# Optimization experiments

Hardware: AMD Instinct MI355X
Metric: run time of the kernel (lower is better)

The kernel has to match this reference:

```python
import jax, jax.numpy as jnp
from jax import lax
import numpy as np

B, T, I, H, L, O = 256, 200, 32, 512, 2, 7
EPS = 1e-12


def setup_inputs() -> dict:
    key = jax.random.key(0)
    ks = jax.random.split(key, 11)
    s = 0.05
    return {
        "x": jax.random.normal(ks[0], (B, T, I), dtype=jnp.float32),
        "w_ih0": jax.random.normal(ks[1], (4 * H, I), dtype=jnp.float32) * s,
        "w_hh0": jax.random.normal(ks[2], (4 * H, H), dtype=jnp.float32) * s,
        "b_ih0": jax.random.normal(ks[3], (4 * H,), dtype=jnp.float32) * s,
        "b_hh0": jax.random.normal(ks[4], (4 * H,), dtype=jnp.float32) * s,
        "w_ih1": jax.random.normal(ks[5], (4 * H, H), dtype=jnp.float32) * s,
        "w_hh1": jax.random.normal(ks[6], (4 * H, H), dtype=jnp.float32) * s,
        "b_ih1": jax.random.normal(ks[7], (4 * H,), dtype=jnp.float32) * s,
        "b_hh1": jax.random.normal(ks[8], (4 * H,), dtype=jnp.float32) * s,
        "w_fc": jax.random.normal(ks[9], (O, H), dtype=jnp.float32) * s,
        "b_fc": jax.random.normal(ks[10], (O,), dtype=jnp.float32) * s,
    }


def _lstm_layer(x_tbi, w_ih, w_hh, b_ih, b_hh):
    # x_tbi: [T, B, in]; PyTorch gate order i, f, g, o
    b = b_ih + b_hh
    hdim = w_hh.shape[1]
    batch = x_tbi.shape[1]
    # precompute input projections for all timesteps (one big GEMM)
    xg = jnp.einsum('tbi,gi->tbg', x_tbi, w_ih) + b  # [T, B, 4H]

    def step(carry, xgt):
        h, c = carry
        g = xgt + h @ w_hh.T
        i, f, gg, o = jnp.split(g, 4, axis=-1)
        c = jax.nn.sigmoid(f) * c + jax.nn.sigmoid(i) * jnp.tanh(gg)
        h = jax.nn.sigmoid(o) * jnp.tanh(c)
        return (h, c), h

    h0 = jnp.zeros((batch, hdim), x_tbi.dtype)
    (_, _), hs = lax.scan(step, (h0, h0), xg)
    return hs  # [T, B, H]


def reference(x, w_ih0, w_hh0, b_ih0, b_hh0, w_ih1, w_hh1, b_ih1, b_hh1, w_fc, b_fc):
    xt = jnp.transpose(x, (1, 0, 2))  # [T, B, I]
    h1 = _lstm_layer(xt, w_ih0, w_hh0, b_ih0, b_hh0)
    h2 = _lstm_layer(h1, w_ih1, w_hh1, b_ih1, b_hh1)
    last = h2[-1]  # [B, H] = output[:, -1, :]
    y = last @ w_fc.T + b_fc  # [B, O]
    p = jax.nn.sigmoid(y[:, :3])
    rt = jnp.tanh(y[:, 3:])
    # F.normalize(p=2, dim=1, eps=1e-12)
    r = rt / jnp.maximum(jnp.linalg.norm(rt, axis=1, keepdims=True), EPS)
    return (p, r)
```

## Files before the change

kernel.cpp:

```cpp
#include <hip/hip_runtime.h>
#include <hip/hip_bf16.h>

#define TSEQ  200
#define BATCH 256
#define INDIM 32
#define HID   512
#define GATES 2048

typedef __bf16 bf16x8 __attribute__((ext_vector_type(8)));
typedef float  f32x4  __attribute__((ext_vector_type(4)));
typedef unsigned long long u64;

static constexpr size_t OFF_PW_IH0 = 0;
static constexpr size_t OFF_PW_HH0 = 0x20000;
static constexpr size_t OFF_PW_IH1 = 0x220000;
static constexpr size_t OFF_PW_HH1 = 0x420000;
static constexpr size_t OFF_B0     = 0x620000;
static constexpr size_t OFF_B1     = 0x622000;
static constexpr size_t OFF_H1     = 0x624000;
static constexpr size_t OFF_H2     = 0x724000;
static constexpr size_t OFF_CTR    = 0x7A4000;
static constexpr size_t OFF_H2P    = 0x7A6000;
static constexpr size_t ZERO_OFF   = OFF_H1;
static constexpr size_t ZERO_LEN   = OFF_H2P + 0x80000 - OFF_H1;

__device__ __forceinline__ float sigm(float v) { return 1.f / (1.f + __expf(-v)); }

__device__ __forceinline__ float tanh_fast(float v) {
    float e = __expf(-2.0f * fabsf(v));
    float t = (1.0f - e) / (1.0f + e);
    return copysignf(t, v);
}

__device__ __forceinline__ bf16x8 as_bf16x8(f32x4 v) {
    union { f32x4 f; bf16x8 b; } u; u.f = v; return u.b;
}

__device__ __forceinline__ bf16x8 load16_coh(const bf16x8* p) {
    bf16x8 v;
    asm volatile("global_load_dwordx4 %0, %1, off sc0 sc1"
                 : "=v"(v) : "v"(p) : "memory");
    return v;
}

__device__ __forceinline__ void store16_coh(void* p, u64 v0, u64 v1) {
    union { u64 u[2]; f32x4 f; } cv; cv.u[0] = v0; cv.u[1] = v1;
    asm volatile("global_store_dwordx4 %0, %1, off sc0 sc1"
                 :: "v"(p), "v"(cv.f) : "memory");
}

__device__ __forceinline__ unsigned load_flag_coh(const unsigned* p) {
    unsigned v;
    asm volatile("global_load_dword %0, %1, off sc0 sc1\n\t"
                 "s_waitcnt vmcnt(0)"
                 : "=v"(v) : "v"(p) : "memory");
    return v;
}

__global__ void pack_w(const float* __restrict__ W, __bf16* __restrict__ out, int ktlog2)
{
    int tid = blockIdx.x * 256 + threadIdx.x;
    int K = 32 << ktlog2;
    int j    = tid & 7;
    int lane = (tid >> 3) & 63;
    int rest = tid >> 9;
    int kt   = rest & ((1 << ktlog2) - 1);
    int r2   = rest >> ktlog2;
    int lnt  = r2 & 7;
    int bn   = r2 >> 3;
    int type = lnt >> 1, half = lnt & 1;
    int g    = type * 512 + bn * 32 + half * 16 + (lane & 15);
    int kcol = kt * 32 + (lane >> 4) * 8 + j;
    out[tid] = (__bf16)W[g * K + kcol];
}

__global__ void bias_comb(const float* __restrict__ a0, const float* __restrict__ a1,
                          const float* __restrict__ a2, const float* __restrict__ a3,
                          float* __restrict__ o0, float* __restrict__ o1)
{
    int tid = blockIdx.x * 256 + threadIdx.x;
    if (tid < GATES) { o0[tid] = a0[tid] + a1[tid]; o1[tid] = a2[tid] + a3[tid]; }
}

__global__ __launch_bounds__(256, 1) void lstm_persist(const float* __restrict__ x,
                                                       const float* __restrict__ wfc,
                                                       const float* __restrict__ bfc,
                                                       char* __restrict__ ws,
                                                       float* __restrict__ out)
{
    const int layer = blockIdx.x >> 7;
    const int lb    = blockIdx.x & 127;
    const int mtp   = lb >> 4;
    const int bn    = lb & 15;
    const int wid   = threadIdx.x >> 6;
    const int half  = wid & 1;
    const int kh    = wid >> 1;
    const int lane  = threadIdx.x & 63;
    const int q     = lane >> 4;
    const int c16   = lane & 15;
    unsigned* flg   = (unsigned*)(ws + OFF_CTR) + (size_t)mtp * 64;

    __shared__ float  red[2][64][33];
    __shared__ __bf16 htr[1024];
    __shared__ bf16x8 stg[2][2][16][64];

    const float* bias = (const float*)(ws + (layer ? OFF_B1 : OFF_B0));
    const int hidx = bn * 32 + half * 16 + c16;
    const float bi  = bias[hidx];
    const float bff = bias[512 + hidx];
    const float bg  = bias[1024 + hidx];
    const float bo  = bias[1536 + hidx];

    const bf16x8* __restrict__ pBx = (const bf16x8*)(ws + OFF_PW_IH0);
    const bf16x8* __restrict__ pBh = (const bf16x8*)(ws + OFF_PW_HH0);
    const bf16x8* __restrict__ pB1 = (const bf16x8*)(ws + OFF_PW_IH1);
    const bf16x8* __restrict__ pB2 = (const bf16x8*)(ws + OFF_PW_HH1);
    float* __restrict__ h2p = (float*)(ws + OFF_H2P);

    f32x4 Bw[64];
    f32x4 Bx[4];
    if (layer == 0) {
        #pragma unroll
        for (int j = 0; j < 8; ++j)
            #pragma unroll
            for (int ty = 0; ty < 4; ++ty)
                Bw[j * 4 + ty] = *(const f32x4*)&pBh[((bn * 8 + ty * 2 + half) * 16 + kh * 8 + j) * 64 + lane];
        #pragma unroll
        for (int ty = 0; ty < 4; ++ty)
            Bx[ty] = *(const f32x4*)&pBx[(bn * 8 + ty * 2 + half) * 64 + lane];
    } else {
        const bf16x8* __restrict__ pW = kh ? pB2 : pB1;
        #pragma unroll
        for (int j = 0; j < 16; ++j)
            #pragma unroll
            for (int ty = 0; ty < 4; ++ty)
                Bw[j * 4 + ty] = *(const f32x4*)&pW[((bn * 8 + ty * 2 + half) * 16 + j) * 64 + lane];
    }

    float creg[8] = {0.f,0.f,0.f,0.f,0.f,0.f,0.f,0.f};

    for (int k = 0; k <= TSEQ; ++k) {
        const bool active = layer ? (k >= 1) : (k < TSEQ);
        if (active) {
            const int t = k - layer;
            f32x4 acc[2][4] = {};

            const size_t h1rd = OFF_H1 + (size_t)((k + 3) & 3) * 0x40000;

            if (layer == 0) {
                const bf16x8* __restrict__ pA = (const bf16x8*)(ws + h1rd);
                bf16x8 tmp0[8];
                #pragma unroll
                for (int j = 0; j < 8; ++j)
                    tmp0[j] = load16_coh(&pA[((mtp * 2 + half) * 16 + kh * 8 + j) * 64 + lane]);
                bf16x8 ax[2];
                if (kh == 0) {
                    #pragma unroll
                    for (int m = 0; m < 2; ++m) {
                        const int b = (mtp * 2 + m) * 16 + c16;
                        const float* xp = x + ((size_t)b * TSEQ + t) * INDIM + q * 8;
                        float4 xlo = *(const float4*)xp;
                        float4 xhi = *(const float4*)(xp + 4);
                        ax[m][0] = (__bf16)xlo.x; ax[m][1] = (__bf16)xlo.y;
                        ax[m][2] = (__bf16)xlo.z; ax[m][3] = (__bf16)xlo.w;
                        ax[m][4] = (__bf16)xhi.x; ax[m][5] = (__bf16)xhi.y;
                        ax[m][6] = (__bf16)xhi.z; ax[m][7] = (__bf16)xhi.w;
                    }
                }
                asm volatile("s_waitcnt vmcnt(0)" ::: "memory");
                __builtin_amdgcn_sched_barrier(0);
                #pragma unroll
                for (int j = 0; j < 8; ++j)
                    stg[kh][half][j][lane] = tmp0[j];
                __syncthreads();
                bf16x8 af[16];
                #pragma unroll
                for (int j = 0; j < 8; ++j) {
                    af[j]     = stg[kh][0][j][lane];
                    af[8 + j] = stg[kh][1][j][lane];
                }
                if (kh == 0) {
                    #pragma unroll
                    for (int m = 0; m < 2; ++m)
                        #pragma unroll
                        for (int ty = 0; ty < 4; ++ty)
                            acc[m][ty] = __builtin_amdgcn_mfma_f32_16x16x32_bf16(ax[m], as_bf16x8(Bx[ty]), acc[m][ty], 0, 0, 0);
                }
                #pragma unroll
                for (int j = 0; j < 8; ++j) {
                    #pragma unroll
                    for (int ty = 0; ty < 4; ++ty) {
                        acc[0][ty] = __builtin_amdgcn_mfma_f32_16x16x32_bf16(af[j],     as_bf16x8(Bw[j * 4 + ty]), acc[0][ty], 0, 0, 0);
                        acc[1][ty] = __builtin_amdgcn_mfma_f32_16x16x32_bf16(af[8 + j], as_bf16x8(Bw[j * 4 + ty]), acc[1][ty], 0, 0, 0);
                    }
                }
            } else {
                const bf16x8* __restrict__ pA = kh
                    ? (const bf16x8*)(ws + OFF_H2 + (size_t)((k + 1) & 1) * 0x40000)
                    : (const bf16x8*)(ws + h1rd);
                bf16x8 tmp[16];
                #pragma unroll
                for (int j = 0; j < 16; ++j)
                    tmp[j] = load16_coh(&pA[((mtp * 2 + half) * 16 + j) * 64 + lane]);
                asm volatile("s_waitcnt vmcnt(0)" ::: "memory");
                __builtin_amdgcn_sched_barrier(0);
                #pragma unroll
                for (int j = 0; j < 16; ++j)
                    stg[kh][half][j][lane] = tmp[j];
                __syncthreads();
                bf16x8 a0[16], a1[16];
                #pragma unroll
                for (int j = 0; j < 8; ++j) {
                    a0[j]     = stg[kh][0][j][lane];
                    a0[8 + j] = stg[kh][1][j][lane];
                    a1[j]     = stg[kh][0][8 + j][lane];
                    a1[8 + j] = stg[kh][1][8 + j][lane];
                }
                #pragma unroll
                for (int j = 0; j < 8; ++j) {
                    #pragma unroll
                    for (int ty = 0; ty < 4; ++ty) {
                        acc[0][ty] = __builtin_amdgcn_mfma_f32_16x16x32_bf16(a0[j],     as_bf16x8(Bw[j * 4 + ty]), acc[0][ty], 0, 0, 0);
                        acc[1][ty] = __builtin_amdgcn_mfma_f32_16x16x32_bf16(a0[8 + j], as_bf16x8(Bw[j * 4 + ty]), acc[1][ty], 0, 0, 0);
                    }
                }
                #pragma unroll
                for (int j = 0; j < 8; ++j) {
                    #pragma unroll
                    for (int ty = 0; ty < 4; ++ty) {
                        acc[0][ty] = __builtin_amdgcn_mfma_f32_16x16x32_bf16(a1[j],     as_bf16x8(Bw[(8 + j) * 4 + ty]), acc[0][ty], 0, 0, 0);
                        acc[1][ty] = __builtin_amdgcn_mfma_f32_16x16x32_bf16(a1[8 + j], as_bf16x8(Bw[(8 + j) * 4 + ty]), acc[1][ty], 0, 0, 0);
                    }
                }
            }

            if (kh == 1) {
                #pragma unroll
                for (int m = 0; m < 2; ++m)
                    #pragma unroll
                    for (int ty = 0; ty < 4; ++ty)
                        #pragma unroll
                        for (int r = 0; r < 4; ++r)
                            red[half][lane][m * 16 + ty * 4 + r] = acc[m][ty][r];
            }
            __syncthreads();

            if (kh == 0) {
                __bf16* __restrict__ hout = (__bf16*)(ws + (layer
                    ? OFF_H2 + (size_t)(k & 1) * 0x40000
                    : OFF_H1 + (size_t)(k & 3) * 0x40000));
                #pragma unroll
                for (int m = 0; m < 2; ++m) {
                    #pragma unroll
                    for (int r = 0; r < 4; ++r) {
                        float pi = acc[m][0][r] + red[half][lane][m * 16 + r]      + bi;
                        float pf = acc[m][1][r] + red[half][lane][m * 16 + 4 + r]  + bff;
                        float pg = acc[m][2][r] + red[half][lane][m * 16 + 8 + r]  + bg;
                        float po = acc[m][3][r] + red[half][lane][m * 16 + 12 + r] + bo;
                        float cn = sigm(pf) * creg[m * 4 + r] + sigm(pi) * tanh_fast(pg);
                        float hn = sigm(po) * tanh_fast(cn);
                        creg[m * 4 + r] = cn;
                        htr[half * 512 + (m * 16 + q * 4 + r) * 16 + c16] = (__bf16)hn;
                        if (layer == 1 && k == TSEQ) {
                            const int b = (mtp * 2 + m) * 16 + q * 4 + r;
                            __hip_atomic_store(&h2p[b * HID + hidx], hn,
                                               __ATOMIC_RELAXED, __HIP_MEMORY_SCOPE_AGENT);
                        }
                    }
                }
                const int bt   = lane >> 5;
                const int qa1  = (lane >> 4) & 1;
                const int b15r = lane & 15;
                const u64* lp = (const u64*)&htr[half * 512 + (bt * 16 + b15r) * 16 + qa1 * 8];
                u64 v0 = lp[0], v1 = lp[1];
                const int f = (((mtp * 2 + bt) * 16) + bn) * 64 + (half * 2 + qa1) * 16 + b15r;
                u64* gp = (u64*)hout + (size_t)f * 2;
                store16_coh(gp, v0, v1);
            }
        }

        asm volatile("s_waitcnt vmcnt(0)" ::: "memory");
        __syncthreads();
        if (threadIdx.x == 0)
            __hip_atomic_store(flg + layer * 16 + bn, (unsigned)(k + 1),
                               __ATOMIC_RELAXED, __HIP_MEMORY_SCOPE_AGENT);
        if (threadIdx.x < 32) {
            const int need = (layer == 0 && threadIdx.x >= 16 && k < TSEQ) ? (k - 1) : (k + 1);
            while ((int)load_flag_coh(flg + threadIdx.x) < need)
                __builtin_amdgcn_s_sleep(1);
        }
        __syncthreads();
    }

    if (threadIdx.x < 64) {
        const int b = mtp * 32 + layer * 16 + bn;
        const float* h = h2p + b * HID;
        float hv[8];
        #pragma unroll
        for (int j = 0; j < 8; ++j)
            hv[j] = __hip_atomic_load(&h[lane * 8 + j], __ATOMIC_RELAXED, __HIP_MEMORY_SCOPE_AGENT);
        float y[7];
        #pragma unroll
        for (int o = 0; o < 7; ++o) {
            const float* wrow = wfc + o * HID;
            float s = 0.f;
            #pragma unroll
            for (int j = 0; j < 8; ++j) s += hv[j] * wrow[lane * 8 + j];
            #pragma unroll
            for (int off = 32; off >= 1; off >>= 1) s += __shfl_down(s, off);
            y[o] = s;
        }
        if (lane == 0) {
            out[b * 3 + 0] = sigm(y[0] + bfc[0]);
            out[b * 3 + 1] = sigm(y[1] + bfc[1]);
            out[b * 3 + 2] = sigm(y[2] + bfc[2]);
            float r0 = tanh_fast(y[3] + bfc[3]);
            float r1 = tanh_fast(y[4] + bfc[4]);
            float r2 = tanh_fast(y[5] + bfc[5]);
            float r3 = tanh_fast(y[6] + bfc[6]);
            float n = sqrtf(r0 * r0 + r1 * r1 + r2 * r2 + r3 * r3);
            n = fmaxf(n, 1e-12f);
            out[768 + b * 4 + 0] = r0 / n;
            out[768 + b * 4 + 1] = r1 / n;
            out[768 + b * 4 + 2] = r2 / n;
            out[768 + b * 4 + 3] = r3 / n;
        }
    }
}

extern "C" void kernel_launch(void* const* d_in, const int* in_sizes, int n_in,
                              void* d_out, int out_size, void* d_ws, size_t ws_size,
                              hipStream_t stream)
{
    const float* x    = (const float*)d_in[0];
    const float* wih0 = (const float*)d_in[1];
    const float* whh0 = (const float*)d_in[2];
    const float* bih0 = (const float*)d_in[3];
    const float* bhh0 = (const float*)d_in[4];
    const float* wih1 = (const float*)d_in[5];
    const float* whh1 = (const float*)d_in[6];
    const float* bih1 = (const float*)d_in[7];
    const float* bhh1 = (const float*)d_in[8];
    const float* wfc  = (const float*)d_in[9];
    const float* bfc  = (const float*)d_in[10];
    char* ws = (char*)d_ws;

    hipMemsetAsync(ws + ZERO_OFF, 0, ZERO_LEN, stream);

    pack_w<<<256,  256, 0, stream>>>(wih0, (__bf16*)(ws + OFF_PW_IH0), 0);
    pack_w<<<4096, 256, 0, stream>>>(whh0, (__bf16*)(ws + OFF_PW_HH0), 4);
    pack_w<<<4096, 256, 0, stream>>>(wih1, (__bf16*)(ws + OFF_PW_IH1), 4);
    pack_w<<<4096, 256, 0, stream>>>(whh1, (__bf16*)(ws + OFF_PW_HH1), 4);
    bias_comb<<<8, 256, 0, stream>>>(bih0, bhh0, bih1, bhh1,
                                     (float*)(ws + OFF_B0), (float*)(ws + OFF_B1));

    lstm_persist<<<256, 256, 0, stream>>>(x, wfc, bfc, ws, (float*)d_out);
}
```

Baseline: 1.433 ms.

## Replace per-step global barrier with tagged-data dataflow sync between LSTM blocks

Drops the per-timestep all-block flag barrier. Each 8-byte granule of the exchanged hidden-state buffers now carries a 16-bit step tag, and consumers spin on the data itself until every tag matches the expected step. Flags survive only as a lighter consumer-progress check that throttles overwriting of the 4-slot ring buffers, and layer-1 reads of h2 now use a 4-slot ring. This is meant to remove the barrier's round-trip latency on the recurrent critical path. In exchange the payload grows by half, 64-bit atomic loads replace 128-bit loads, there is extra packing work, and the polling is more complex.

```diff
diff --git a/kernel.cpp b/kernel.cpp
--- a/kernel.cpp
+++ b/kernel.cpp
@@ -17,12 +17,13 @@
 static constexpr size_t OFF_PW_HH1 = 0x420000;
 static constexpr size_t OFF_B0     = 0x620000;
 static constexpr size_t OFF_B1     = 0x622000;
-static constexpr size_t OFF_H1     = 0x624000;
-static constexpr size_t OFF_H2     = 0x724000;
-static constexpr size_t OFF_CTR    = 0x7A4000;
-static constexpr size_t OFF_H2P    = 0x7A6000;
-static constexpr size_t ZERO_OFF   = OFF_H1;
-static constexpr size_t ZERO_LEN   = OFF_H2P + 0x80000 - OFF_H1;
+static constexpr size_t SLOT_SZ    = 0x60000;
+static constexpr size_t OFF_RH1    = 0x20000;
+static constexpr size_t OFF_RH2    = 0x1A0000;
+static constexpr size_t OFF_CTR    = 0x624000;
+static constexpr size_t OFF_H2P    = 0x626000;
+static constexpr size_t ZERO_OFF   = OFF_CTR;
+static constexpr size_t ZERO_LEN   = OFF_H2P + 0x80000 - OFF_CTR;
 
 __device__ __forceinline__ float sigm(float v) { return 1.f / (1.f + __expf(-v)); }
 
@@ -36,19 +37,19 @@
     union { f32x4 f; bf16x8 b; } u; u.f = v; return u.b;
 }
 
-__device__ __forceinline__ bf16x8 load16_coh(const bf16x8* p) {
-    bf16x8 v;
-    asm volatile("global_load_dwordx4 %0, %1, off sc0 sc1"
+__device__ __forceinline__ u64 ld_gran(const void* p) {
+    return __hip_atomic_load((const u64*)p, __ATOMIC_RELAXED, __HIP_MEMORY_SCOPE_AGENT);
+}
+__device__ __forceinline__ void st_gran(void* p, u64 v) {
+    __hip_atomic_store((u64*)p, v, __ATOMIC_RELAXED, __HIP_MEMORY_SCOPE_AGENT);
+}
+
+__device__ __forceinline__ unsigned load_flag_async(const unsigned* p) {
+    unsigned v;
+    asm volatile("global_load_dword %0, %1, off sc0 sc1"
                  : "=v"(v) : "v"(p) : "memory");
     return v;
 }
-
-__device__ __forceinline__ void store16_coh(void* p, u64 v0, u64 v1) {
-    union { u64 u[2]; f32x4 f; } cv; cv.u[0] = v0; cv.u[1] = v1;
-    asm volatile("global_store_dwordx4 %0, %1, off sc0 sc1"
-                 :: "v"(p), "v"(cv.f) : "memory");
-}
-
 __device__ __forceinline__ unsigned load_flag_coh(const unsigned* p) {
     unsigned v;
     asm volatile("global_load_dword %0, %1, off sc0 sc1\n\t"
@@ -136,79 +137,105 @@
             for (int ty = 0; ty < 4; ++ty)
                 Bw[j * 4 + ty] = *(const f32x4*)&pW[((bn * 8 + ty * 2 + half) * 16 + j) * 64 + lane];
     }
+    asm volatile("s_waitcnt vmcnt(0)" ::: "memory");
+    __builtin_amdgcn_sched_barrier(0);
+    __syncthreads();
+    if (threadIdx.x == 0)
+        __hip_atomic_store(flg + layer * 16 + bn, 1u, __ATOMIC_RELAXED,
+                           __HIP_MEMORY_SCOPE_AGENT);
 
     float creg[8] = {0.f,0.f,0.f,0.f,0.f,0.f,0.f,0.f};
+
+    auto stage_frags = [&](const char* sb, int kt0, int NF, int want) {
+        const int abase = (mtp * 2 + half) * 16 + kt0;
+        const u64 w = (u64)(unsigned)want;
+        u64 g0[16], g1[16], g2[16];
+        #pragma unroll
+        for (int j = 0; j < 16; ++j) if (j < NF) {
+            const char* p = sb + ((size_t)(abase + j) * 64 + lane) * 24;
+            g0[j] = ld_gran(p); g1[j] = ld_gran(p + 8); g2[j] = ld_gran(p + 16);
+        }
+        while (true) {
+            bool ok = true;
+            #pragma unroll
+            for (int j = 0; j < 16; ++j) if (j < NF)
+                ok &= ((g0[j] >> 48) == w) & ((g1[j] >> 48) == w) & ((g2[j] >> 48) == w);
+            if (__all(ok)) break;
+            __builtin_amdgcn_s_sleep(1);
+            #pragma unroll
+            for (int j = 0; j < 16; ++j) if (j < NF) {
+                const char* p = sb + ((size_t)(abase + j) * 64 + lane) * 24;
+                if ((g0[j] >> 48) != w) g0[j] = ld_gran(p);
+                if ((g1[j] >> 48) != w) g1[j] = ld_gran(p + 8);
+                if ((g2[j] >> 48) != w) g2[j] = ld_gran(p + 16);
+            }
+        }
+        #pragma unroll
+        for (int j = 0; j < 16; ++j) if (j < NF) {
+            union { unsigned short s[8]; bf16x8 b; } cv;
+            cv.s[0] = (unsigned short)g0[j];
+            cv.s[1] = (unsigned short)(g0[j] >> 16);
+            cv.s[2] = (unsigned short)(g0[j] >> 32);
+            cv.s[3] = (unsigned short)g1[j];
+            cv.s[4] = (unsigned short)(g1[j] >> 16);
+            cv.s[5] = (unsigned short)(g1[j] >> 32);
+            cv.s[6] = (unsigned short)g2[j];
+            cv.s[7] = (unsigned short)(g2[j] >> 16);
+            stg[kh][half][j][lane] = cv.b;
+        }
+    };
 
     for (int k = 0; k <= TSEQ; ++k) {
         const bool active = layer ? (k >= 1) : (k < TSEQ);
         if (active) {
             const int t = k - layer;
             f32x4 acc[2][4] = {};
-
-            const size_t h1rd = OFF_H1 + (size_t)((k + 3) & 3) * 0x40000;
+            const bool recur = (layer == 1) || (k > 0);
+            const bool h2ok  = (layer == 0) || (k > 1);
+
+            const char* rd_h1 = ws + OFF_RH1 + (size_t)((k + 3) & 3) * SLOT_SZ;
+            const char* rd_h2 = ws + OFF_RH2 + (size_t)((k + 2) & 3) * SLOT_SZ;
+
+            unsigned pf = 0;
+            if (kh == 0 && lane < 32) pf = load_flag_async(flg + lane);
 
             if (layer == 0) {
-                const bf16x8* __restrict__ pA = (const bf16x8*)(ws + h1rd);
-                bf16x8 tmp0[8];
-                #pragma unroll
-                for (int j = 0; j < 8; ++j)
-                    tmp0[j] = load16_coh(&pA[((mtp * 2 + half) * 16 + kh * 8 + j) * 64 + lane]);
-                bf16x8 ax[2];
-                if (kh == 0) {
-                    #pragma unroll
-                    for (int m = 0; m < 2; ++m) {
-                        const int b = (mtp * 2 + m) * 16 + c16;
-                        const float* xp = x + ((size_t)b * TSEQ + t) * INDIM + q * 8;
-                        float4 xlo = *(const float4*)xp;
-                        float4 xhi = *(const float4*)(xp + 4);
-                        ax[m][0] = (__bf16)xlo.x; ax[m][1] = (__bf16)xlo.y;
-                        ax[m][2] = (__bf16)xlo.z; ax[m][3] = (__bf16)xlo.w;
-                        ax[m][4] = (__bf16)xhi.x; ax[m][5] = (__bf16)xhi.y;
-                        ax[m][6] = (__bf16)xhi.z; ax[m][7] = (__bf16)xhi.w;
-                    }
-                }
-                asm volatile("s_waitcnt vmcnt(0)" ::: "memory");
-                __builtin_amdgcn_sched_barrier(0);
-                #pragma unroll
-                for (int j = 0; j < 8; ++j)
-                    stg[kh][half][j][lane] = tmp0[j];
-                __syncthreads();
-                bf16x8 af[16];
-                #pragma unroll
-                for (int j = 0; j < 8; ++j) {
-                    af[j]     = stg[kh][0][j][lane];
-                    af[8 + j] = stg[kh][1][j][lane];
-                }
-                if (kh == 0) {
-                    #pragma unroll
-                    for (int m = 0; m < 2; ++m)
-                        #pragma unroll
-                        for (int ty = 0; ty < 4; ++ty)
-                            acc[m][ty] = __builtin_amdgcn_mfma_f32_16x16x32_bf16(ax[m], as_bf16x8(Bx[ty]), acc[m][ty], 0, 0, 0);
-                }
-                #pragma unroll
-                for (int j = 0; j < 8; ++j) {
-                    #pragma unroll
-                    for (int ty = 0; ty < 4; ++ty) {
-                        acc[0][ty] = __builtin_amdgcn_mfma_f32_16x16x32_bf16(af[j],     as_bf16x8(Bw[j * 4 + ty]), acc[0][ty], 0, 0, 0);
-                        acc[1][ty] = __builtin_amdgcn_mfma_f32_16x16x32_bf16(af[8 + j], as_bf16x8(Bw[j * 4 + ty]), acc[1][ty], 0, 0, 0);
-                    }
-                }
+                if (recur) stage_frags(rd_h1, kh * 8, 8, k);
             } else {
-                const bf16x8* __restrict__ pA = kh
-                    ? (const bf16x8*)(ws + OFF_H2 + (size_t)((k + 1) & 1) * 0x40000)
-                    : (const bf16x8*)(ws + h1rd);
-                bf16x8 tmp[16];
-                #pragma unroll
-                for (int j = 0; j < 16; ++j)
-                    tmp[j] = load16_coh(&pA[((mtp * 2 + half) * 16 + j) * 64 + lane]);
-                asm volatile("s_waitcnt vmcnt(0)" ::: "memory");
-                __builtin_amdgcn_sched_barrier(0);
-                #pragma unroll
-                for (int j = 0; j < 16; ++j)
-                    stg[kh][half][j][lane] = tmp[j];
-                __syncthreads();
-                bf16x8 a0[16], a1[16];
+                if (kh == 0) stage_frags(rd_h1, 0, 16, k);
+                else if (h2ok) stage_frags(rd_h2, 0, 16, k - 1);
+            }
+
+            bf16x8 ax[2];
+            if (layer == 0 && kh == 0) {
+                #pragma unroll
+                for (int m = 0; m < 2; ++m) {
+                    const int b = (mtp * 2 + m) * 16 + c16;
+                    const float* xp = x + ((size_t)b * TSEQ + t) * INDIM + q * 8;
+                    float4 xlo = *(const float4*)xp;
+                    float4 xhi = *(const float4*)(xp + 4);
+                    ax[m][0] = (__bf16)xlo.x; ax[m][1] = (__bf16)xlo.y;
+                    ax[m][2] = (__bf16)xlo.z; ax[m][3] = (__bf16)xlo.w;
+                    ax[m][4] = (__bf16)xhi.x; ax[m][5] = (__bf16)xhi.y;
+                    ax[m][6] = (__bf16)xhi.z; ax[m][7] = (__bf16)xhi.w;
+                }
+            }
+
+            __syncthreads();
+            if (threadIdx.x == 0)
+                __hip_atomic_store(flg + layer * 16 + bn, (unsigned)(k + 2),
+                                   __ATOMIC_RELAXED, __HIP_MEMORY_SCOPE_AGENT);
+
+            bf16x8 a0[16], a1[16];
+            if (layer == 0) {
+                if (recur) {
+                    #pragma unroll
+                    for (int j = 0; j < 8; ++j) {
+                        a0[j]     = stg[kh][0][j][lane];
+                        a0[8 + j] = stg[kh][1][j][lane];
+                    }
+                }
+            } else if (kh == 0 || h2ok) {
                 #pragma unroll
                 for (int j = 0; j < 8; ++j) {
                     a0[j]     = stg[kh][0][j][lane];
@@ -216,6 +243,28 @@
                     a1[j]     = stg[kh][0][8 + j][lane];
                     a1[8 + j] = stg[kh][1][8 + j][lane];
                 }
+            }
+            __syncthreads();
+
+            if (layer == 0) {
+                if (kh == 0) {
+                    #pragma unroll
+                    for (int m = 0; m < 2; ++m)
+                        #pragma unroll
+                        for (int ty = 0; ty < 4; ++ty)
+                            acc[m][ty] = __builtin_amdgcn_mfma_f32_16x16x32_bf16(ax[m], as_bf16x8(Bx[ty]), acc[m][ty], 0, 0, 0);
+                }
+                if (recur) {
+                    #pragma unroll
+                    for (int j = 0; j < 8; ++j) {
+                        #pragma unroll
+                        for (int ty = 0; ty < 4; ++ty) {
+                            acc[0][ty] = __builtin_amdgcn_mfma_f32_16x16x32_bf16(a0[j],     as_bf16x8(Bw[j * 4 + ty]), acc[0][ty], 0, 0, 0);
+                            acc[1][ty] = __builtin_amdgcn_mfma_f32_16x16x32_bf16(a0[8 + j], as_bf16x8(Bw[j * 4 + ty]), acc[1][ty], 0, 0, 0);
+                        }
+                    }
+                }
+            } else if (kh == 0 || h2ok) {
                 #pragma unroll
                 for (int j = 0; j < 8; ++j) {
                     #pragma unroll
@@ -246,18 +295,15 @@
             __syncthreads();
 
             if (kh == 0) {
-                __bf16* __restrict__ hout = (__bf16*)(ws + (layer
-                    ? OFF_H2 + (size_t)(k & 1) * 0x40000
-                    : OFF_H1 + (size_t)(k & 3) * 0x40000));
                 #pragma unroll
                 for (int m = 0; m < 2; ++m) {
                     #pragma unroll
                     for (int r = 0; r < 4; ++r) {
-                        float pi = acc[m][0][r] + red[half][lane][m * 16 + r]      + bi;
-                        float pf = acc[m][1][r] + red[half][lane][m * 16 + 4 + r]  + bff;
-                        float pg = acc[m][2][r] + red[half][lane][m * 16 + 8 + r]  + bg;
-                        float po = acc[m][3][r] + red[half][lane][m * 16 + 12 + r] + bo;
-                        float cn = sigm(pf) * creg[m * 4 + r] + sigm(pi) * tanh_fast(pg);
+                        float pi  = acc[m][0][r] + red[half][lane][m * 16 + r]      + bi;
+                        float pff = acc[m][1][r] + red[half][lane][m * 16 + 4 + r]  + bff;
+                        float pg  = acc[m][2][r] + red[half][lane][m * 16 + 8 + r]  + bg;
+                        float po  = acc[m][3][r] + red[half][lane][m * 16 + 12 + r] + bo;
+                        float cn = sigm(pff) * creg[m * 4 + r] + sigm(pi) * tanh_fast(pg);
                         float hn = sigm(po) * tanh_fast(cn);
                         creg[m * 4 + r] = cn;
                         htr[half * 512 + (m * 16 + q * 4 + r) * 16 + c16] = (__bf16)hn;
@@ -268,29 +314,49 @@
                         }
                     }
                 }
+                asm volatile("s_waitcnt vmcnt(0)" ::: "memory");
+                __builtin_amdgcn_sched_barrier(0);
+                {
+                    int need = k - 1; if (need < 1) need = 1;
+                    bool pok = (lane < 32) ? ((int)pf >= need) : true;
+                    while (!__all(pok)) {
+                        __builtin_amdgcn_s_sleep(1);
+                        if (lane < 32) pf = load_flag_coh(flg + lane);
+                        pok = (lane < 32) ? ((int)pf >= need) : true;
+                    }
+                }
+                char* hout = ws + (layer
+                    ? OFF_RH2 + (size_t)((k + 3) & 3) * SLOT_SZ
+                    : OFF_RH1 + (size_t)(k & 3) * SLOT_SZ);
+                const u64 tag48 = (u64)(unsigned)(layer ? k : k + 1) << 48;
                 const int bt   = lane >> 5;
                 const int qa1  = (lane >> 4) & 1;
                 const int b15r = lane & 15;
                 const u64* lp = (const u64*)&htr[half * 512 + (bt * 16 + b15r) * 16 + qa1 * 8];
                 u64 v0 = lp[0], v1 = lp[1];
                 const int f = (((mtp * 2 + bt) * 16) + bn) * 64 + (half * 2 + qa1) * 16 + b15r;
-                u64* gp = (u64*)hout + (size_t)f * 2;
-                store16_coh(gp, v0, v1);
-            }
-        }
-
-        asm volatile("s_waitcnt vmcnt(0)" ::: "memory");
-        __syncthreads();
-        if (threadIdx.x == 0)
-            __hip_atomic_store(flg + layer * 16 + bn, (unsigned)(k + 1),
-                               __ATOMIC_RELAXED, __HIP_MEMORY_SCOPE_AGENT);
-        if (threadIdx.x < 32) {
-            const int need = (layer == 0 && threadIdx.x >= 16 && k < TSEQ) ? (k - 1) : (k + 1);
-            while ((int)load_flag_coh(flg + threadIdx.x) < need)
-                __builtin_amdgcn_s_sleep(1);
-        }
-        __syncthreads();
+                char* gp = hout + (size_t)f * 24;
+                st_gran(gp,      (v0 & 0xFFFFFFFFFFFFull) | tag48);
+                st_gran(gp + 8,  ((v0 >> 48) | ((v1 & 0xFFFFFFFFull) << 16)) | tag48);
+                st_gran(gp + 16, ((v1 >> 32) & 0xFFFFFFFFull) | tag48);
+            }
+        } else {
+            if (threadIdx.x == 0)
+                __hip_atomic_store(flg + layer * 16 + bn, (unsigned)(k + 2),
+                                   __ATOMIC_RELAXED, __HIP_MEMORY_SCOPE_AGENT);
+        }
     }
+
+    asm volatile("s_waitcnt vmcnt(0)" ::: "memory");
+    __syncthreads();
+    if (threadIdx.x == 0)
+        __hip_atomic_store(flg + layer * 16 + bn, (unsigned)(TSEQ + 3),
+                           __ATOMIC_RELAXED, __HIP_MEMORY_SCOPE_AGENT);
+    if (threadIdx.x < 32) {
+        while ((int)load_flag_coh(flg + threadIdx.x) < TSEQ + 3)
+            __builtin_amdgcn_s_sleep(1);
+    }
+    __syncthreads();
 
     if (threadIdx.x < 64) {
         const int b = mtp * 32 + layer * 16 + bn;
```

After: 5.327 ms. 3.72x slower.

## Split per-step barrier into consume/produce flags with 4-deep layer-2 ring

Applied to the files above, without the earlier changes.

Replaces the single end-of-step global barrier with two flag sets. A produce flag is posted after a block writes its h slice. A consume flag is posted once the block has staged its inputs into LDS. Each block now waits only on the specific producers it depends on, and checks consumer progress only just before overwriting a ring slot. The layer-2 hidden state buffer becomes a 4-slot ring to allow more slack, and the x load is issued before the wait. The final FC stage reads the last h2 from the bf16 ring instead of a separate fp32 copy. This adds complexity and risks ordering bugs, and the final FC now uses bf16 h instead of fp32.

```diff
diff --git a/kernel.cpp b/kernel.cpp
--- a/kernel.cpp
+++ b/kernel.cpp
@@ -19,10 +19,9 @@
 static constexpr size_t OFF_B1     = 0x622000;
 static constexpr size_t OFF_H1     = 0x624000;
 static constexpr size_t OFF_H2     = 0x724000;
-static constexpr size_t OFF_CTR    = 0x7A4000;
-static constexpr size_t OFF_H2P    = 0x7A6000;
+static constexpr size_t OFF_CTR    = 0x824000;
 static constexpr size_t ZERO_OFF   = OFF_H1;
-static constexpr size_t ZERO_LEN   = OFF_H2P + 0x80000 - OFF_H1;
+static constexpr size_t ZERO_LEN   = 0x825000 - OFF_H1;
 
 __device__ __forceinline__ float sigm(float v) { return 1.f / (1.f + __expf(-v)); }
 
@@ -55,6 +54,17 @@
                  "s_waitcnt vmcnt(0)"
                  : "=v"(v) : "v"(p) : "memory");
     return v;
+}
+
+__device__ __forceinline__ unsigned load_flag_async(const unsigned* p) {
+    unsigned v;
+    asm volatile("global_load_dword %0, %1, off sc0 sc1"
+                 : "=v"(v) : "v"(p) : "memory");
+    return v;
+}
+
+__device__ __forceinline__ void post_flag(unsigned* p, unsigned v) {
+    __hip_atomic_store(p, v, __ATOMIC_RELAXED, __HIP_MEMORY_SCOPE_AGENT);
 }
 
 __global__ void pack_w(const float* __restrict__ W, __bf16* __restrict__ out, int ktlog2)
@@ -98,7 +108,8 @@
     const int lane  = threadIdx.x & 63;
     const int q     = lane >> 4;
     const int c16   = lane & 15;
-    unsigned* flg   = (unsigned*)(ws + OFF_CTR) + (size_t)mtp * 64;
+    unsigned* cflg  = (unsigned*)(ws + OFF_CTR) + (size_t)mtp * 128;
+    unsigned* pflg  = cflg + 64;
 
     __shared__ float  red[2][64][33];
     __shared__ __bf16 htr[1024];
@@ -115,7 +126,6 @@
     const bf16x8* __restrict__ pBh = (const bf16x8*)(ws + OFF_PW_HH0);
     const bf16x8* __restrict__ pB1 = (const bf16x8*)(ws + OFF_PW_IH1);
     const bf16x8* __restrict__ pB2 = (const bf16x8*)(ws + OFF_PW_HH1);
-    float* __restrict__ h2p = (float*)(ws + OFF_H2P);
 
     f32x4 Bw[64];
     f32x4 Bx[4];
@@ -139,13 +149,38 @@
 
     float creg[8] = {0.f,0.f,0.f,0.f,0.f,0.f,0.f,0.f};
 
+    auto wait_flags16 = [&](const unsigned* base, int need) {
+        bool ok = (lane < 16) ? ((int)load_flag_coh(base + lane) >= need) : true;
+        while (!__all(ok)) {
+            __builtin_amdgcn_s_sleep(1);
+            ok = (lane < 16) ? ((int)load_flag_coh(base + lane) >= need) : true;
+        }
+    };
+
     for (int k = 0; k <= TSEQ; ++k) {
         const bool active = layer ? (k >= 1) : (k < TSEQ);
         if (active) {
             const int t = k - layer;
             f32x4 acc[2][4] = {};
-
             const size_t h1rd = OFF_H1 + (size_t)((k + 3) & 3) * 0x40000;
+
+            float4 xlo[2], xhi[2];
+            if (layer == 0 && kh == 0) {
+                #pragma unroll
+                for (int m = 0; m < 2; ++m) {
+                    const int b = (mtp * 2 + m) * 16 + c16;
+                    const float* xp = x + ((size_t)b * TSEQ + t) * INDIM + q * 8;
+                    xlo[m] = *(const float4*)xp;
+                    xhi[m] = *(const float4*)(xp + 4);
+                }
+            }
+
+            if (layer == 0) {
+                if (k >= 1) wait_flags16(pflg, k);
+            } else {
+                if (kh == 0) wait_flags16(pflg, k);
+                else if (k >= 2) wait_flags16(pflg + 16, k);
+            }
 
             if (layer == 0) {
                 const bf16x8* __restrict__ pA = (const bf16x8*)(ws + h1rd);
@@ -153,50 +188,14 @@
                 #pragma unroll
                 for (int j = 0; j < 8; ++j)
                     tmp0[j] = load16_coh(&pA[((mtp * 2 + half) * 16 + kh * 8 + j) * 64 + lane]);
-                bf16x8 ax[2];
-                if (kh == 0) {
-                    #pragma unroll
-                    for (int m = 0; m < 2; ++m) {
-                        const int b = (mtp * 2 + m) * 16 + c16;
-                        const float* xp = x + ((size_t)b * TSEQ + t) * INDIM + q * 8;
-                        float4 xlo = *(const float4*)xp;
-                        float4 xhi = *(const float4*)(xp + 4);
-                        ax[m][0] = (__bf16)xlo.x; ax[m][1] = (__bf16)xlo.y;
-                        ax[m][2] = (__bf16)xlo.z; ax[m][3] = (__bf16)xlo.w;
-                        ax[m][4] = (__bf16)xhi.x; ax[m][5] = (__bf16)xhi.y;
-                        ax[m][6] = (__bf16)xhi.z; ax[m][7] = (__bf16)xhi.w;
-                    }
-                }
                 asm volatile("s_waitcnt vmcnt(0)" ::: "memory");
                 __builtin_amdgcn_sched_barrier(0);
                 #pragma unroll
                 for (int j = 0; j < 8; ++j)
                     stg[kh][half][j][lane] = tmp0[j];
-                __syncthreads();
-                bf16x8 af[16];
-                #pragma unroll
-                for (int j = 0; j < 8; ++j) {
-                    af[j]     = stg[kh][0][j][lane];
-                    af[8 + j] = stg[kh][1][j][lane];
-                }
-                if (kh == 0) {
-                    #pragma unroll
-                    for (int m = 0; m < 2; ++m)
-                        #pragma unroll
-                        for (int ty = 0; ty < 4; ++ty)
-                            acc[m][ty] = __builtin_amdgcn_mfma_f32_16x16x32_bf16(ax[m], as_bf16x8(Bx[ty]), acc[m][ty], 0, 0, 0);
-                }
-                #pragma unroll
-                for (int j = 0; j < 8; ++j) {
-                    #pragma unroll
-                    for (int ty = 0; ty < 4; ++ty) {
-                        acc[0][ty] = __builtin_amdgcn_mfma_f32_16x16x32_bf16(af[j],     as_bf16x8(Bw[j * 4 + ty]), acc[0][ty], 0, 0, 0);
-                        acc[1][ty] = __builtin_amdgcn_mfma_f32_16x16x32_bf16(af[8 + j], as_bf16x8(Bw[j * 4 + ty]), acc[1][ty], 0, 0, 0);
-                    }
-                }
             } else {
                 const bf16x8* __restrict__ pA = kh
-                    ? (const bf16x8*)(ws + OFF_H2 + (size_t)((k + 1) & 1) * 0x40000)
+                    ? (const bf16x8*)(ws + OFF_H2 + (size_t)((k + 3) & 3) * 0x40000)
                     : (const bf16x8*)(ws + h1rd);
                 bf16x8 tmp[16];
                 #pragma unroll
@@ -207,8 +206,31 @@
                 #pragma unroll
                 for (int j = 0; j < 16; ++j)
                     stg[kh][half][j][lane] = tmp[j];
-                __syncthreads();
-                bf16x8 a0[16], a1[16];
+            }
+            bf16x8 ax[2];
+            if (layer == 0 && kh == 0) {
+                #pragma unroll
+                for (int m = 0; m < 2; ++m) {
+                    ax[m][0] = (__bf16)xlo[m].x; ax[m][1] = (__bf16)xlo[m].y;
+                    ax[m][2] = (__bf16)xlo[m].z; ax[m][3] = (__bf16)xlo[m].w;
+                    ax[m][4] = (__bf16)xhi[m].x; ax[m][5] = (__bf16)xhi[m].y;
+                    ax[m][6] = (__bf16)xhi[m].z; ax[m][7] = (__bf16)xhi[m].w;
+                }
+            }
+            __syncthreads();
+            if (threadIdx.x == 0)
+                post_flag(cflg + layer * 16 + bn, (unsigned)(k + 1));
+            unsigned pf = 0;
+            if (kh == 0 && lane < 32) pf = load_flag_async(cflg + lane);
+
+            bf16x8 a0[16], a1[16];
+            if (layer == 0) {
+                #pragma unroll
+                for (int j = 0; j < 8; ++j) {
+                    a0[j]     = stg[kh][0][j][lane];
+                    a0[8 + j] = stg[kh][1][j][lane];
+                }
+            } else {
                 #pragma unroll
                 for (int j = 0; j < 8; ++j) {
                     a0[j]     = stg[kh][0][j][lane];
@@ -216,6 +238,17 @@
                     a1[j]     = stg[kh][0][8 + j][lane];
                     a1[8 + j] = stg[kh][1][8 + j][lane];
                 }
+            }
+            __syncthreads();
+
+            if (layer == 0) {
+                if (kh == 0) {
+                    #pragma unroll
+                    for (int m = 0; m < 2; ++m)
+                        #pragma unroll
+                        for (int ty = 0; ty < 4; ++ty)
+                            acc[m][ty] = __builtin_amdgcn_mfma_f32_16x16x32_bf16(ax[m], as_bf16x8(Bx[ty]), acc[m][ty], 0, 0, 0);
+                }
                 #pragma unroll
                 for (int j = 0; j < 8; ++j) {
                     #pragma unroll
@@ -224,6 +257,15 @@
                         acc[1][ty] = __builtin_amdgcn_mfma_f32_16x16x32_bf16(a0[8 + j], as_bf16x8(Bw[j * 4 + ty]), acc[1][ty], 0, 0, 0);
                     }
                 }
+            } else {
+                #pragma unroll
+                for (int j = 0; j < 8; ++j) {
+                    #pragma unroll
+                    for (int ty = 0; ty < 4; ++ty) {
+                        acc[0][ty] = __builtin_amdgcn_mfma_f32_16x16x32_bf16(a0[j],     as_bf16x8(Bw[j * 4 + ty]), acc[0][ty], 0, 0, 0);
+                        acc[1][ty] = __builtin_amdgcn_mfma_f32_16x16x32_bf16(a0[8 + j], as_bf16x8(Bw[j * 4 + ty]), acc[1][ty], 0, 0, 0);
+                    }
+                }
                 #pragma unroll
                 for (int j = 0; j < 8; ++j) {
                     #pragma unroll
@@ -246,28 +288,38 @@
             __syncthreads();
 
             if (kh == 0) {
-                __bf16* __restrict__ hout = (__bf16*)(ws + (layer
-                    ? OFF_H2 + (size_t)(k & 1) * 0x40000
-                    : OFF_H1 + (size_t)(k & 3) * 0x40000));
                 #pragma unroll
                 for (int m = 0; m < 2; ++m) {
                     #pragma unroll
                     for (int r = 0; r < 4; ++r) {
-                        float pi = acc[m][0][r] + red[half][lane][m * 16 + r]      + bi;
-                        float pf = acc[m][1][r] + red[half][lane][m * 16 + 4 + r]  + bff;
-                        float pg = acc[m][2][r] + red[half][lane][m * 16 + 8 + r]  + bg;
-                        float po = acc[m][3][r] + red[half][lane][m * 16 + 12 + r] + bo;
-                        float cn = sigm(pf) * creg[m * 4 + r] + sigm(pi) * tanh_fast(pg);
+                        float pi  = acc[m][0][r] + red[half][lane][m * 16 + r]      + bi;
+                        float pff = acc[m][1][r] + red[half][lane][m * 16 + 4 + r]  + bff;
+                        float pg  = acc[m][2][r] + red[half][lane][m * 16 + 8 + r]  + bg;
+                        float po  = acc[m][3][r] + red[half][lane][m * 16 + 12 + r] + bo;
+                        float cn = sigm(pff) * creg[m * 4 + r] + sigm(pi) * tanh_fast(pg);
                         float hn = sigm(po) * tanh_fast(cn);
                         creg[m * 4 + r] = cn;
                         htr[half * 512 + (m * 16 + q * 4 + r) * 16 + c16] = (__bf16)hn;
-                        if (layer == 1 && k == TSEQ) {
-                            const int b = (mtp * 2 + m) * 16 + q * 4 + r;
-                            __hip_atomic_store(&h2p[b * HID + hidx], hn,
-                                               __ATOMIC_RELAXED, __HIP_MEMORY_SCOPE_AGENT);
-                        }
                     }
                 }
+                asm volatile("s_waitcnt vmcnt(0)" ::: "memory");
+                __builtin_amdgcn_sched_barrier(0);
+                {
+                    const int need = k - 2;
+                    bool pok = (lane < 32)
+                        ? ((layer == 1 && lane < 16) ? true : ((int)pf >= need))
+                        : true;
+                    while (!__all(pok)) {
+                        __builtin_amdgcn_s_sleep(1);
+                        if (lane < 32) pf = load_flag_coh(cflg + lane);
+                        pok = (lane < 32)
+                            ? ((layer == 1 && lane < 16) ? true : ((int)pf >= need))
+                            : true;
+                    }
+                }
+                __bf16* __restrict__ hout = (__bf16*)(ws + (layer
+                    ? OFF_H2 + (size_t)(k & 3) * 0x40000
+                    : OFF_H1 + (size_t)(k & 3) * 0x40000));
                 const int bt   = lane >> 5;
                 const int qa1  = (lane >> 4) & 1;
                 const int b15r = lane & 15;
@@ -276,29 +328,36 @@
                 const int f = (((mtp * 2 + bt) * 16) + bn) * 64 + (half * 2 + qa1) * 16 + b15r;
                 u64* gp = (u64*)hout + (size_t)f * 2;
                 store16_coh(gp, v0, v1);
+                asm volatile("s_waitcnt vmcnt(0)" ::: "memory");
+            }
+            __syncthreads();
+            if (threadIdx.x == 0)
+                post_flag(pflg + layer * 16 + bn, (unsigned)(k + 1));
+        } else {
+            if (threadIdx.x == 0) {
+                post_flag(cflg + layer * 16 + bn, (unsigned)(k + 1));
+                post_flag(pflg + layer * 16 + bn, (unsigned)(k + 1));
             }
         }
-
+    }
+
+    if (threadIdx.x < 64) {
+        {
+            bool ok = (lane < 16) ? ((int)load_flag_coh(pflg + 16 + lane) >= TSEQ + 1) : true;
+            while (!__all(ok)) {
+                __builtin_amdgcn_s_sleep(1);
+                ok = (lane < 16) ? ((int)load_flag_coh(pflg + 16 + lane) >= TSEQ + 1) : true;
+            }
+        }
+        const int b = mtp * 32 + layer * 16 + bn;
+        const bf16x8* ring = (const bf16x8*)(ws + OFF_H2 + (size_t)(TSEQ & 3) * 0x40000);
+        const int a = ((b >> 4) * 16 + (lane >> 2)) * 64 + ((lane & 3) << 4) + (b & 15);
+        bf16x8 hb = load16_coh(ring + a);
         asm volatile("s_waitcnt vmcnt(0)" ::: "memory");
-        __syncthreads();
-        if (threadIdx.x == 0)
-            __hip_atomic_store(flg + layer * 16 + bn, (unsigned)(k + 1),
-                               __ATOMIC_RELAXED, __HIP_MEMORY_SCOPE_AGENT);
-        if (threadIdx.x < 32) {
-            const int need = (layer == 0 && threadIdx.x >= 16 && k < TSEQ) ? (k - 1) : (k + 1);
-            while ((int)load_flag_coh(flg + threadIdx.x) < need)
-                __builtin_amdgcn_s_sleep(1);
-        }
-        __syncthreads();
-    }
-
-    if (threadIdx.x < 64) {
-        const int b = mtp * 32 + layer * 16 + bn;
-        const float* h = h2p + b * HID;
+        __builtin_amdgcn_sched_barrier(0);
         float hv[8];
         #pragma unroll
-        for (int j = 0; j < 8; ++j)
-            hv[j] = __hip_atomic_load(&h[lane * 8 + j], __ATOMIC_RELAXED, __HIP_MEMORY_SCOPE_AGENT);
+        for (int j = 0; j < 8; ++j) hv[j] = (float)hb[j];
         float y[7];
         #pragma unroll
         for (int o = 0; o < 7; ++o) {
```

Measured after the change: 1.955 ms. 36.4% more time.
